# Kernel tuning notes

Measured on AMD Instinct MI355X. Metric: run time of the kernel, lower is better.

## Reference

```python
import jax, jax.numpy as jnp
import numpy as np


def setup_inputs() -> dict:
    key = jax.random.key(0)
    ks = jax.random.split(key, 6)
    B, V, T, Fin = 16, 12288, 4, 64
    Kv, Kt, Fout = 4, 4, 64
    NNZ = 9 * V  # ~8 neighbors + self loop per vertex (HEALPix)
    inputs = jax.random.normal(ks[0], (B, V, T, Fin), dtype=jnp.float32)
    std = np.sqrt(2.0 / (Fin * Kv * Kt))
    weight = jax.random.normal(ks[1], (Fin, Kv, Kt, Fout), dtype=jnp.float32) * std
    bias = jnp.zeros((Fout,), dtype=jnp.float32)
    lap_rows = jax.random.randint(ks[2], (NNZ,), 0, V, dtype=jnp.int32)
    lap_cols = jax.random.randint(ks[3], (NNZ,), 0, V, dtype=jnp.int32)
    # small values so the Chebyshev recurrence stays numerically tame
    lap_vals = jax.random.normal(ks[4], (NNZ,), dtype=jnp.float32) * 0.1
    return {"inputs": inputs, "weight": weight, "bias": bias,
            "lap_vals": lap_vals, "lap_rows": lap_rows, "lap_cols": lap_cols}


def _cheb_conv_temp(inputs, weight, lap_vals, lap_rows, lap_cols):
    B, V, T, Fin = inputs.shape
    Fin_w, Kv, Kt, Fout = weight.shape
    # x0: [V, T*Fin*B] matching torch permute(1,2,3,0).view
    x0 = jnp.transpose(inputs, (1, 2, 3, 0)).reshape(V, T * Fin * B)

    def spmm(x):  # sparse laplacian @ x via gather + segment_sum
        return jax.ops.segment_sum(lap_vals[:, None] * x[lap_cols], lap_rows,
                                   num_segments=V)

    xs = [x0]
    if Kv > 1:
        x1 = spmm(x0)
        xs.append(x1)
        for _ in range(2, Kv):
            x2 = 2.0 * spmm(x1) - x0
            xs.append(x2)
            x0, x1 = x1, x2
    x = jnp.stack(xs, axis=0).reshape(Kv, V, T, Fin, B)
    # contraction aligns flattened (Fin,Kv,T) of x with (Fin,Kv,Kt) of weight
    return jnp.einsum('kvtfb,fkto->bvo', x, weight)


def reference(inputs, weight, bias, lap_vals, lap_rows, lap_cols):
    out = _cheb_conv_temp(inputs, weight, lap_vals, lap_rows, lap_cols)
    return out + bias
```

## Files before the change

kernel.cpp:

```cpp
#include <hip/hip_runtime.h>

#define V_N 12288
#define B_N 16
#define TF_N 256
#define ROW2 1024
#define FOUT 64
#define TPB_TILES 4

typedef __attribute__((ext_vector_type(8))) short short8;
typedef __attribute__((ext_vector_type(4))) float f32x4;

__device__ __forceinline__ unsigned short f2bf(float x){
  unsigned u = __float_as_uint(x);
  return (unsigned short)((u + 0x7FFFu + ((u >> 16) & 1u)) >> 16);
}
__device__ __forceinline__ float bf2f(unsigned short h){
  return __uint_as_float(((unsigned)h) << 16);
}

__global__ void k_zero(int* __restrict__ p, int n){
  int i = blockIdx.x * 256 + threadIdx.x;
  if (i < n) p[i] = 0;
}

__global__ void k_hist(const int* __restrict__ rows, int* __restrict__ cnt, int nnz){
  int i = blockIdx.x * 256 + threadIdx.x;
  if (i < nnz) atomicAdd(&cnt[rows[i]], 1);
}

__global__ void k_scan(const int* __restrict__ cnt, int* __restrict__ rp){
  __shared__ int part[256];
  __shared__ int base[257];
  int t = threadIdx.x;
  const int per = V_N / 256;
  int4 c[12];
  #pragma unroll
  for (int i = 0; i < 12; ++i) c[i] = *(const int4*)(cnt + t * per + i * 4);
  int s = 0;
  #pragma unroll
  for (int i = 0; i < 12; ++i) s += c[i].x + c[i].y + c[i].z + c[i].w;
  part[t] = s;
  __syncthreads();
  if (t == 0){
    int run = 0;
    for (int i = 0; i < 256; ++i){ base[i] = run; run += part[i]; }
    base[256] = run;
  }
  __syncthreads();
  int run = base[t];
  #pragma unroll
  for (int i = 0; i < 12; ++i){
    int4 o;
    o.x = run; run += c[i].x;
    o.y = run; run += c[i].y;
    o.z = run; run += c[i].z;
    o.w = run; run += c[i].w;
    *(int4*)(rp + t * per + i * 4) = o;
  }
  if (t == 255) rp[V_N] = run;
}

__global__ void k_scatter(const int* __restrict__ rows, const int* __restrict__ cols,
                          const float* __restrict__ vals, const int* __restrict__ rp,
                          int* __restrict__ cur, int* __restrict__ cols_s,
                          float* __restrict__ vals_s, int nnz){
  int i = blockIdx.x * 256 + threadIdx.x;
  if (i < nnz){
    int r = rows[i];
    int pos = rp[r] + atomicAdd(&cur[r], 1);
    cols_s[pos] = cols[i];
    vals_s[pos] = vals[i];
  }
}

__global__ void k_convw(const float* __restrict__ w, unsigned short* __restrict__ wb){
  int i = blockIdx.x * 256 + threadIdx.x;
  int j = i & 7;
  int l = (i >> 3) & 63;
  int n = (i >> 9) & 3;
  int s = (i >> 11) & 7;
  int k = (i >> 14) & 3;
  int kk = s * 32 + ((l >> 4) << 3) + j;
  int t = kk >> 6, f = kk & 63;
  int o = (n << 4) + (l & 15);
  wb[i] = f2bf(w[((f * 4 + k) * 4 + t) * 64 + o]);
}

__global__ __launch_bounds__(256, 2) void k_proj(
                       const float* __restrict__ in, const unsigned short* __restrict__ wb,
                       unsigned short* __restrict__ y0, unsigned short* __restrict__ y1,
                       unsigned short* __restrict__ y2, unsigned short* __restrict__ y3){
  __shared__ unsigned short As[2][32 * 256];
  int t = threadIdx.x;
  int lane = t & 63;
  int k    = t >> 6;
  int colL = lane & 15, rg = lane >> 4;

  int tile0 = blockIdx.x * TPB_TILES;

  float4 r[8];
  {
    int vb = tile0 >> 4, b = tile0 & 15;
    const float* src = in + ((size_t)b * V_N + vb * 32) * TF_N;
    #pragma unroll
    for (int i = 0; i < 8; ++i) r[i] = *(const float4*)(src + i * 1024 + t * 4);
  }

  short8 W[8][4];
  {
    const unsigned short* wk = wb + k * 16384 + lane * 8;
    #pragma unroll
    for (int s = 0; s < 8; ++s)
      #pragma unroll
      for (int n = 0; n < 4; ++n)
        W[s][n] = *(const short8*)(wk + (((s * 4 + n)) << 9));
  }
  unsigned short* yk = (k == 0) ? y0 : (k == 1) ? y1 : (k == 2) ? y2 : y3;

  for (int ti = 0; ti < TPB_TILES; ++ti){
    int ft = tile0 + ti;
    char* lds = (char*)As[ti & 1];
    #pragma unroll
    for (int i = 0; i < 8; ++i){
      int flat = i * 1024 + t * 4;
      int row = flat >> 8;
      int c2  = (flat & 255) * 2;
      unsigned long long pk =  (unsigned long long)f2bf(r[i].x)
                            | ((unsigned long long)f2bf(r[i].y) << 16)
                            | ((unsigned long long)f2bf(r[i].z) << 32)
                            | ((unsigned long long)f2bf(r[i].w) << 48);
      *(unsigned long long*)(lds + ((row * 512 + c2) ^ ((row & 7) << 4))) = pk;
    }
    if (ti + 1 < TPB_TILES){
      int ft1 = ft + 1;
      int vb = ft1 >> 4, b = ft1 & 15;
      const float* src = in + ((size_t)b * V_N + vb * 32) * TF_N;
      #pragma unroll
      for (int i = 0; i < 8; ++i) r[i] = *(const float4*)(src + i * 1024 + t * 4);
    }
    __syncthreads();

    f32x4 acc[2][4];
    #pragma unroll
    for (int mt = 0; mt < 2; ++mt)
      #pragma unroll
      for (int n = 0; n < 4; ++n) acc[mt][n] = (f32x4){0.f, 0.f, 0.f, 0.f};

    #pragma unroll
    for (int s = 0; s < 8; ++s){
      int c2 = rg * 16 + s * 64;
      short8 a0 = *(const short8*)(lds + (( colL       * 512 + c2) ^ ((colL & 7) << 4)));
      short8 a1 = *(const short8*)(lds + (((16 + colL) * 512 + c2) ^ ((colL & 7) << 4)));
      #pragma unroll
      for (int n = 0; n < 4; ++n){
        acc[0][n] = __builtin_amdgcn_mfma_f32_16x16x32_bf16(a0, W[s][n], acc[0][n], 0, 0, 0);
        acc[1][n] = __builtin_amdgcn_mfma_f32_16x16x32_bf16(a1, W[s][n], acc[1][n], 0, 0, 0);
      }
    }
    {
      int vb = ft >> 4, b = ft & 15, v0 = vb * 32;
      #pragma unroll
      for (int mt = 0; mt < 2; ++mt)
        #pragma unroll
        for (int q = 0; q < 4; ++q){
          int v = v0 + mt * 16 + rg * 4 + q;
          unsigned lo = (unsigned)f2bf(acc[mt][0][q]) | ((unsigned)f2bf(acc[mt][1][q]) << 16);
          unsigned hi = (unsigned)f2bf(acc[mt][2][q]) | ((unsigned)f2bf(acc[mt][3][q]) << 16);
          uint2 pk = {lo, hi};
          *(uint2*)(yk + (size_t)v * ROW2 + b * 64 + colL * 4) = pk;
        }
    }
    __syncthreads();
  }
}

__global__ void k_spmm2(const unsigned short* __restrict__ src,
                        const unsigned short* __restrict__ addA,
                        const unsigned short* __restrict__ subB,
                        unsigned short* __restrict__ dst,
                        const int* __restrict__ rp, const int* __restrict__ cols,
                        const float* __restrict__ vals, float alpha){
  int lane = threadIdx.x & 63;
  int r = blockIdx.x * 4 + (threadIdx.x >> 6);
  int j0 = lane * 16;
  float acc[16];
  #pragma unroll
  for (int p = 0; p < 16; ++p) acc[p] = 0.f;
  int beg = rp[r], end = rp[r + 1];
  for (int i = beg; i < end; ++i){
    float val = vals[i];
    int c = cols[i];
    const unsigned short* srow = src + (size_t)c * ROW2 + j0;
    short8 a0 = *(const short8*)srow;
    short8 a1 = *(const short8*)(srow + 8);
    #pragma unroll
    for (int p = 0; p < 8; ++p) acc[p]     += val * bf2f((unsigned short)a0[p]);
    #pragma unroll
    for (int p = 0; p < 8; ++p) acc[p + 8] += val * bf2f((unsigned short)a1[p]);
  }
  const unsigned short* arow = addA + (size_t)r * ROW2 + j0;
  short8 q0 = *(const short8*)arow;
  short8 q1 = *(const short8*)(arow + 8);
  #pragma unroll
  for (int p = 0; p < 8; ++p) acc[p]     = alpha * acc[p]     + bf2f((unsigned short)q0[p]);
  #pragma unroll
  for (int p = 0; p < 8; ++p) acc[p + 8] = alpha * acc[p + 8] + bf2f((unsigned short)q1[p]);
  if (subB){
    const unsigned short* brow = subB + (size_t)r * ROW2 + j0;
    short8 s0 = *(const short8*)brow;
    short8 s1 = *(const short8*)(brow + 8);
    #pragma unroll
    for (int p = 0; p < 8; ++p) acc[p]     -= bf2f((unsigned short)s0[p]);
    #pragma unroll
    for (int p = 0; p < 8; ++p) acc[p + 8] -= bf2f((unsigned short)s1[p]);
  }
  unsigned short* drow = dst + (size_t)r * ROW2 + j0;
  short8 o0, o1;
  #pragma unroll
  for (int p = 0; p < 8; ++p) o0[p] = (short)f2bf(acc[p]);
  #pragma unroll
  for (int p = 0; p < 8; ++p) o1[p] = (short)f2bf(acc[p + 8]);
  *(short8*)drow = o0;
  *(short8*)(drow + 8) = o1;
}

__global__ void k_final(const unsigned short* __restrict__ src,
                        const unsigned short* __restrict__ y0,
                        const unsigned short* __restrict__ b2,
                        const float* __restrict__ bias,
                        float* __restrict__ out,
                        const int* __restrict__ rp, const int* __restrict__ cols,
                        const float* __restrict__ vals){
  int lane = threadIdx.x & 63;
  int v = blockIdx.x * 4 + (threadIdx.x >> 6);
  int j0 = lane * 16;
  float acc[16];
  #pragma unroll
  for (int p = 0; p < 16; ++p) acc[p] = 0.f;
  int beg = rp[v], end = rp[v + 1];
  for (int i = beg; i < end; ++i){
    float val = vals[i];
    int c = cols[i];
    const unsigned short* srow = src + (size_t)c * ROW2 + j0;
    short8 a0 = *(const short8*)srow;
    short8 a1 = *(const short8*)(srow + 8);
    #pragma unroll
    for (int p = 0; p < 8; ++p) acc[p]     += val * bf2f((unsigned short)a0[p]);
    #pragma unroll
    for (int p = 0; p < 8; ++p) acc[p + 8] += val * bf2f((unsigned short)a1[p]);
  }
  const unsigned short* yrow = y0 + (size_t)v * ROW2 + j0;
  const unsigned short* brow = b2 + (size_t)v * ROW2 + j0;
  short8 q0 = *(const short8*)yrow;
  short8 q1 = *(const short8*)(yrow + 8);
  short8 s0 = *(const short8*)brow;
  short8 s1 = *(const short8*)(brow + 8);
  #pragma unroll
  for (int p = 0; p < 8; ++p) acc[p]     += bf2f((unsigned short)q0[p]) - bf2f((unsigned short)s0[p]);
  #pragma unroll
  for (int p = 0; p < 8; ++p) acc[p + 8] += bf2f((unsigned short)q1[p]) - bf2f((unsigned short)s1[p]);
  int b = lane >> 2;
  int c0 = (lane & 3) * 4;
  float* obase = out + ((size_t)b * V_N + v) * FOUT;
  #pragma unroll
  for (int n = 0; n < 4; ++n){
    float4 bv = *(const float4*)(bias + n * 16 + c0);
    float4 w;
    w.x = acc[0 * 4 + n] + bv.x;
    w.y = acc[1 * 4 + n] + bv.y;
    w.z = acc[2 * 4 + n] + bv.z;
    w.w = acc[3 * 4 + n] + bv.w;
    *(float4*)(obase + n * 16 + c0) = w;
  }
}

extern "C" void kernel_launch(void* const* d_in, const int* in_sizes, int n_in,
                              void* d_out, int out_size, void* d_ws, size_t ws_size,
                              hipStream_t stream) {
  const float* inputs   = (const float*)d_in[0];
  const float* weight   = (const float*)d_in[1];
  const float* bias     = (const float*)d_in[2];
  const float* lap_vals = (const float*)d_in[3];
  const int*   lap_rows = (const int*)d_in[4];
  const int*   lap_cols = (const int*)d_in[5];
  float* out = (float*)d_out;
  int nnz = in_sizes[3];

  char* ws = (char*)d_ws;
  size_t off = 0;
  auto alloc = [&](size_t bytes) -> void* {
    void* p = ws + off;
    off += (bytes + 255) & ~(size_t)255;
    return p;
  };
  const size_t YB = (size_t)V_N * ROW2 * 2;
  unsigned short* y0 = (unsigned short*)alloc(YB);
  unsigned short* y1 = (unsigned short*)alloc(YB);
  unsigned short* y2 = (unsigned short*)alloc(YB);
  unsigned short* y3 = (unsigned short*)alloc(YB);
  unsigned short* c2 = (unsigned short*)alloc(YB);
  unsigned short* c1 = (unsigned short*)alloc(YB);
  unsigned short* wb = (unsigned short*)alloc(65536 * 2);
  int*   cnt   = (int*)alloc(V_N * 4);
  int*   cur   = (int*)alloc(V_N * 4);
  int*   rp    = (int*)alloc((V_N + 1) * 4);
  int*   colss = (int*)alloc((size_t)nnz * 4);
  float* valss = (float*)alloc((size_t)nnz * 4);

  k_zero<<<(2 * V_N + 255) / 256, 256, 0, stream>>>(cnt, 2 * V_N);
  k_hist<<<(nnz + 255) / 256, 256, 0, stream>>>(lap_rows, cnt, nnz);
  k_scan<<<1, 256, 0, stream>>>(cnt, rp);
  k_scatter<<<(nnz + 255) / 256, 256, 0, stream>>>(lap_rows, lap_cols, lap_vals, rp, cur,
                                                   colss, valss, nnz);
  k_convw<<<65536 / 256, 256, 0, stream>>>(weight, wb);
  k_proj<<<(V_N / 32) * B_N / TPB_TILES, 256, 0, stream>>>(inputs, wb, y0, y1, y2, y3);

  k_spmm2<<<V_N / 4, 256, 0, stream>>>(y3, y2, nullptr, c2, rp, colss, valss, 2.0f);
  k_spmm2<<<V_N / 4, 256, 0, stream>>>(c2, y1, y3, c1, rp, colss, valss, 2.0f);
  k_final<<<V_N / 4, 256, 0, stream>>>(c1, y0, c2, bias, out, rp, colss, valss);
}
```

Before: 215.2 us.

## Stream projection inputs directly into LDS and split SpMM rows across two waves

The projection kernel now copies fp32 input tiles from global memory straight into a double-buffered LDS array with the async global_load_lds builtin, using a pre-swizzled source address. The bf16 conversion moves to the LDS read side, which frees the staging registers and lets the next tile's load overlap the current MFMA work. The SpMM and final kernels give each row to two waves of 8 elements per lane instead of one wave of 16, doubling the grid to improve parallelism and latency hiding. The trade-offs are twice the LDS footprint (fp32 tiles), more conversion work per LDS read, and twice as many column and value index loads in the SpMM kernels.

```diff
diff --git a/kernel.cpp b/kernel.cpp
--- a/kernel.cpp
+++ b/kernel.cpp
@@ -90,7 +90,7 @@
                        const float* __restrict__ in, const unsigned short* __restrict__ wb,
                        unsigned short* __restrict__ y0, unsigned short* __restrict__ y1,
                        unsigned short* __restrict__ y2, unsigned short* __restrict__ y3){
-  __shared__ unsigned short As[2][32 * 256];
+  __shared__ float As[2][32 * 256];
   int t = threadIdx.x;
   int lane = t & 63;
   int k    = t >> 6;
@@ -98,12 +98,18 @@
 
   int tile0 = blockIdx.x * TPB_TILES;
 
-  float4 r[8];
   {
     int vb = tile0 >> 4, b = tile0 & 15;
-    const float* src = in + ((size_t)b * V_N + vb * 32) * TF_N;
-    #pragma unroll
-    for (int i = 0; i < 8; ++i) r[i] = *(const float4*)(src + i * 1024 + t * 4);
+    const char* gsrc = (const char*)(in + ((size_t)b * V_N + vb * 32) * TF_N);
+    char* lb = (char*)As[0];
+    #pragma unroll
+    for (int i = 0; i < 8; ++i){
+      int W = i * 4096 + t * 16;
+      int x = ((W >> 10) & 7) << 4;
+      __builtin_amdgcn_global_load_lds(
+          (const __attribute__((address_space(1))) unsigned int*)(gsrc + (W ^ x)),
+          (__attribute__((address_space(3))) unsigned int*)(lb + W), 16, 0, 0);
+    }
   }
 
   short8 W[8][4];
@@ -113,44 +119,53 @@
     for (int s = 0; s < 8; ++s)
       #pragma unroll
       for (int n = 0; n < 4; ++n)
-        W[s][n] = *(const short8*)(wk + (((s * 4 + n)) << 9));
+        W[s][n] = *(const short8*)(wk + ((s * 4 + n) << 9));
   }
   unsigned short* yk = (k == 0) ? y0 : (k == 1) ? y1 : (k == 2) ? y2 : y3;
 
   for (int ti = 0; ti < TPB_TILES; ++ti){
     int ft = tile0 + ti;
-    char* lds = (char*)As[ti & 1];
-    #pragma unroll
-    for (int i = 0; i < 8; ++i){
-      int flat = i * 1024 + t * 4;
-      int row = flat >> 8;
-      int c2  = (flat & 255) * 2;
-      unsigned long long pk =  (unsigned long long)f2bf(r[i].x)
-                            | ((unsigned long long)f2bf(r[i].y) << 16)
-                            | ((unsigned long long)f2bf(r[i].z) << 32)
-                            | ((unsigned long long)f2bf(r[i].w) << 48);
-      *(unsigned long long*)(lds + ((row * 512 + c2) ^ ((row & 7) << 4))) = pk;
-    }
+    __syncthreads();
     if (ti + 1 < TPB_TILES){
       int ft1 = ft + 1;
       int vb = ft1 >> 4, b = ft1 & 15;
-      const float* src = in + ((size_t)b * V_N + vb * 32) * TF_N;
-      #pragma unroll
-      for (int i = 0; i < 8; ++i) r[i] = *(const float4*)(src + i * 1024 + t * 4);
+      const char* gsrc = (const char*)(in + ((size_t)b * V_N + vb * 32) * TF_N);
+      char* lb = (char*)As[(ti + 1) & 1];
+      #pragma unroll
+      for (int i = 0; i < 8; ++i){
+        int W = i * 4096 + t * 16;
+        int x = ((W >> 10) & 7) << 4;
+        __builtin_amdgcn_global_load_lds(
+            (const __attribute__((address_space(1))) unsigned int*)(gsrc + (W ^ x)),
+            (__attribute__((address_space(3))) unsigned int*)(lb + W), 16, 0, 0);
+      }
     }
-    __syncthreads();
-
+
+    const char* lds = (const char*)As[ti & 1];
     f32x4 acc[2][4];
     #pragma unroll
     for (int mt = 0; mt < 2; ++mt)
       #pragma unroll
       for (int n = 0; n < 4; ++n) acc[mt][n] = (f32x4){0.f, 0.f, 0.f, 0.f};
 
+    int xr = (colL & 7) << 4;
     #pragma unroll
     for (int s = 0; s < 8; ++s){
-      int c2 = rg * 16 + s * 64;
-      short8 a0 = *(const short8*)(lds + (( colL       * 512 + c2) ^ ((colL & 7) << 4)));
-      short8 a1 = *(const short8*)(lds + (((16 + colL) * 512 + c2) ^ ((colL & 7) << 4)));
+      int B0 = colL * 1024 + rg * 32 + s * 128;
+      int B1 = (colL + 16) * 1024 + rg * 32 + s * 128;
+      float4 f00 = *(const float4*)(lds + ((B0) ^ xr));
+      float4 f01 = *(const float4*)(lds + ((B0 + 16) ^ xr));
+      float4 f10 = *(const float4*)(lds + ((B1) ^ xr));
+      float4 f11 = *(const float4*)(lds + ((B1 + 16) ^ xr));
+      short8 a0, a1;
+      a0[0] = (short)f2bf(f00.x); a0[1] = (short)f2bf(f00.y);
+      a0[2] = (short)f2bf(f00.z); a0[3] = (short)f2bf(f00.w);
+      a0[4] = (short)f2bf(f01.x); a0[5] = (short)f2bf(f01.y);
+      a0[6] = (short)f2bf(f01.z); a0[7] = (short)f2bf(f01.w);
+      a1[0] = (short)f2bf(f10.x); a1[1] = (short)f2bf(f10.y);
+      a1[2] = (short)f2bf(f10.z); a1[3] = (short)f2bf(f10.w);
+      a1[4] = (short)f2bf(f11.x); a1[5] = (short)f2bf(f11.y);
+      a1[6] = (short)f2bf(f11.z); a1[7] = (short)f2bf(f11.w);
       #pragma unroll
       for (int n = 0; n < 4; ++n){
         acc[0][n] = __builtin_amdgcn_mfma_f32_16x16x32_bf16(a0, W[s][n], acc[0][n], 0, 0, 0);
@@ -170,7 +185,6 @@
           *(uint2*)(yk + (size_t)v * ROW2 + b * 64 + colL * 4) = pk;
         }
     }
-    __syncthreads();
   }
 }
 
@@ -181,47 +195,32 @@
                         const int* __restrict__ rp, const int* __restrict__ cols,
                         const float* __restrict__ vals, float alpha){
   int lane = threadIdx.x & 63;
-  int r = blockIdx.x * 4 + (threadIdx.x >> 6);
-  int j0 = lane * 16;
-  float acc[16];
-  #pragma unroll
-  for (int p = 0; p < 16; ++p) acc[p] = 0.f;
+  int wave = threadIdx.x >> 6;
+  int r = blockIdx.x * 2 + (wave >> 1);
+  int j0 = (wave & 1) * 512 + lane * 8;
+  float acc[8];
+  #pragma unroll
+  for (int p = 0; p < 8; ++p) acc[p] = 0.f;
   int beg = rp[r], end = rp[r + 1];
   for (int i = beg; i < end; ++i){
     float val = vals[i];
     int c = cols[i];
-    const unsigned short* srow = src + (size_t)c * ROW2 + j0;
-    short8 a0 = *(const short8*)srow;
-    short8 a1 = *(const short8*)(srow + 8);
-    #pragma unroll
-    for (int p = 0; p < 8; ++p) acc[p]     += val * bf2f((unsigned short)a0[p]);
-    #pragma unroll
-    for (int p = 0; p < 8; ++p) acc[p + 8] += val * bf2f((unsigned short)a1[p]);
-  }
-  const unsigned short* arow = addA + (size_t)r * ROW2 + j0;
-  short8 q0 = *(const short8*)arow;
-  short8 q1 = *(const short8*)(arow + 8);
-  #pragma unroll
-  for (int p = 0; p < 8; ++p) acc[p]     = alpha * acc[p]     + bf2f((unsigned short)q0[p]);
-  #pragma unroll
-  for (int p = 0; p < 8; ++p) acc[p + 8] = alpha * acc[p + 8] + bf2f((unsigned short)q1[p]);
+    short8 a0 = *(const short8*)(src + (size_t)c * ROW2 + j0);
+    #pragma unroll
+    for (int p = 0; p < 8; ++p) acc[p] += val * bf2f((unsigned short)a0[p]);
+  }
+  short8 q0 = *(const short8*)(addA + (size_t)r * ROW2 + j0);
+  #pragma unroll
+  for (int p = 0; p < 8; ++p) acc[p] = alpha * acc[p] + bf2f((unsigned short)q0[p]);
   if (subB){
-    const unsigned short* brow = subB + (size_t)r * ROW2 + j0;
-    short8 s0 = *(const short8*)brow;
-    short8 s1 = *(const short8*)(brow + 8);
-    #pragma unroll
-    for (int p = 0; p < 8; ++p) acc[p]     -= bf2f((unsigned short)s0[p]);
-    #pragma unroll
-    for (int p = 0; p < 8; ++p) acc[p + 8] -= bf2f((unsigned short)s1[p]);
-  }
-  unsigned short* drow = dst + (size_t)r * ROW2 + j0;
-  short8 o0, o1;
+    short8 s0 = *(const short8*)(subB + (size_t)r * ROW2 + j0);
+    #pragma unroll
+    for (int p = 0; p < 8; ++p) acc[p] -= bf2f((unsigned short)s0[p]);
+  }
+  short8 o0;
   #pragma unroll
   for (int p = 0; p < 8; ++p) o0[p] = (short)f2bf(acc[p]);
-  #pragma unroll
-  for (int p = 0; p < 8; ++p) o1[p] = (short)f2bf(acc[p + 8]);
-  *(short8*)drow = o0;
-  *(short8*)(drow + 8) = o1;
+  *(short8*)(dst + (size_t)r * ROW2 + j0) = o0;
 }
 
 __global__ void k_final(const unsigned short* __restrict__ src,
@@ -232,45 +231,36 @@
                         const int* __restrict__ rp, const int* __restrict__ cols,
                         const float* __restrict__ vals){
   int lane = threadIdx.x & 63;
-  int v = blockIdx.x * 4 + (threadIdx.x >> 6);
-  int j0 = lane * 16;
-  float acc[16];
-  #pragma unroll
-  for (int p = 0; p < 16; ++p) acc[p] = 0.f;
+  int wave = threadIdx.x >> 6;
+  int v = blockIdx.x * 2 + (wave >> 1);
+  int jh = wave & 1;
+  int j0 = jh * 512 + lane * 8;
+  float acc[8];
+  #pragma unroll
+  for (int p = 0; p < 8; ++p) acc[p] = 0.f;
   int beg = rp[v], end = rp[v + 1];
   for (int i = beg; i < end; ++i){
     float val = vals[i];
     int c = cols[i];
-    const unsigned short* srow = src + (size_t)c * ROW2 + j0;
-    short8 a0 = *(const short8*)srow;
-    short8 a1 = *(const short8*)(srow + 8);
-    #pragma unroll
-    for (int p = 0; p < 8; ++p) acc[p]     += val * bf2f((unsigned short)a0[p]);
-    #pragma unroll
-    for (int p = 0; p < 8; ++p) acc[p + 8] += val * bf2f((unsigned short)a1[p]);
-  }
-  const unsigned short* yrow = y0 + (size_t)v * ROW2 + j0;
-  const unsigned short* brow = b2 + (size_t)v * ROW2 + j0;
-  short8 q0 = *(const short8*)yrow;
-  short8 q1 = *(const short8*)(yrow + 8);
-  short8 s0 = *(const short8*)brow;
-  short8 s1 = *(const short8*)(brow + 8);
-  #pragma unroll
-  for (int p = 0; p < 8; ++p) acc[p]     += bf2f((unsigned short)q0[p]) - bf2f((unsigned short)s0[p]);
-  #pragma unroll
-  for (int p = 0; p < 8; ++p) acc[p + 8] += bf2f((unsigned short)q1[p]) - bf2f((unsigned short)s1[p]);
-  int b = lane >> 2;
-  int c0 = (lane & 3) * 4;
-  float* obase = out + ((size_t)b * V_N + v) * FOUT;
+    short8 a0 = *(const short8*)(src + (size_t)c * ROW2 + j0);
+    #pragma unroll
+    for (int p = 0; p < 8; ++p) acc[p] += val * bf2f((unsigned short)a0[p]);
+  }
+  short8 q0 = *(const short8*)(y0 + (size_t)v * ROW2 + j0);
+  short8 s0 = *(const short8*)(b2 + (size_t)v * ROW2 + j0);
+  #pragma unroll
+  for (int p = 0; p < 8; ++p)
+    acc[p] += bf2f((unsigned short)q0[p]) - bf2f((unsigned short)s0[p]);
+  int bb = jh * 8 + (lane >> 3);
+  int cl2 = (lane & 7) * 2;
+  float* obase = out + ((size_t)bb * V_N + v) * FOUT;
   #pragma unroll
   for (int n = 0; n < 4; ++n){
-    float4 bv = *(const float4*)(bias + n * 16 + c0);
-    float4 w;
-    w.x = acc[0 * 4 + n] + bv.x;
-    w.y = acc[1 * 4 + n] + bv.y;
-    w.z = acc[2 * 4 + n] + bv.z;
-    w.w = acc[3 * 4 + n] + bv.w;
-    *(float4*)(obase + n * 16 + c0) = w;
+    int o = n * 16 + cl2;
+    float2 w;
+    w.x = acc[n]     + bias[o];
+    w.y = acc[4 + n] + bias[o + 1];
+    *(float2*)(obase + o) = w;
   }
 }
 
@@ -315,7 +305,7 @@
   k_convw<<<65536 / 256, 256, 0, stream>>>(weight, wb);
   k_proj<<<(V_N / 32) * B_N / TPB_TILES, 256, 0, stream>>>(inputs, wb, y0, y1, y2, y3);
 
-  k_spmm2<<<V_N / 4, 256, 0, stream>>>(y3, y2, nullptr, c2, rp, colss, valss, 2.0f);
-  k_spmm2<<<V_N / 4, 256, 0, stream>>>(c2, y1, y3, c1, rp, colss, valss, 2.0f);
-  k_final<<<V_N / 4, 256, 0, stream>>>(c1, y0, c2, bias, out, rp, colss, valss);
-}
+  k_spmm2<<<V_N / 2, 256, 0, stream>>>(y3, y2, nullptr, c2, rp, colss, valss, 2.0f);
+  k_spmm2<<<V_N / 2, 256, 0, stream>>>(c2, y1, y3, c1, rp, colss, valss, 2.0f);
+  k_final<<<V_N / 2, 256, 0, stream>>>(c1, y0, c2, bias, out, rp, colss, valss);
+}
```

Result: slower. 229.0 us (+6.4%).

## Split SpMM rows across 8 blocks with 2 bf16 elements per lane

Applied to the files above, without the earlier changes.

The SpMM and final kernels now split each 1024-wide bf16 row into 8 slices, so each wave handles 128 columns and each lane 2 elements. The grid grows 8x. This raises parallelism and cuts per-thread register use, hiding gather latency better. In exchange each lane does narrower 4-byte loads, the CSR indices and values are re-read 8 times, and the final output uses scalar scattered stores instead of float4.

```diff
diff --git a/kernel.cpp b/kernel.cpp
--- a/kernel.cpp
+++ b/kernel.cpp
@@ -113,7 +113,7 @@
     for (int s = 0; s < 8; ++s)
       #pragma unroll
       for (int n = 0; n < 4; ++n)
-        W[s][n] = *(const short8*)(wk + (((s * 4 + n)) << 9));
+        W[s][n] = *(const short8*)(wk + ((s * 4 + n) << 9));
   }
   unsigned short* yk = (k == 0) ? y0 : (k == 1) ? y1 : (k == 2) ? y2 : y3;
 
@@ -180,48 +180,30 @@
                         unsigned short* __restrict__ dst,
                         const int* __restrict__ rp, const int* __restrict__ cols,
                         const float* __restrict__ vals, float alpha){
+  int s = blockIdx.x & 7;
   int lane = threadIdx.x & 63;
-  int r = blockIdx.x * 4 + (threadIdx.x >> 6);
-  int j0 = lane * 16;
-  float acc[16];
-  #pragma unroll
-  for (int p = 0; p < 16; ++p) acc[p] = 0.f;
+  int wave = threadIdx.x >> 6;
+  int r = (blockIdx.x >> 3) * 4 + wave;
+  int j0 = s * 128 + lane * 2;
+  float a0 = 0.f, a1 = 0.f;
   int beg = rp[r], end = rp[r + 1];
   for (int i = beg; i < end; ++i){
     float val = vals[i];
     int c = cols[i];
-    const unsigned short* srow = src + (size_t)c * ROW2 + j0;
-    short8 a0 = *(const short8*)srow;
-    short8 a1 = *(const short8*)(srow + 8);
-    #pragma unroll
-    for (int p = 0; p < 8; ++p) acc[p]     += val * bf2f((unsigned short)a0[p]);
-    #pragma unroll
-    for (int p = 0; p < 8; ++p) acc[p + 8] += val * bf2f((unsigned short)a1[p]);
-  }
-  const unsigned short* arow = addA + (size_t)r * ROW2 + j0;
-  short8 q0 = *(const short8*)arow;
-  short8 q1 = *(const short8*)(arow + 8);
-  #pragma unroll
-  for (int p = 0; p < 8; ++p) acc[p]     = alpha * acc[p]     + bf2f((unsigned short)q0[p]);
-  #pragma unroll
-  for (int p = 0; p < 8; ++p) acc[p + 8] = alpha * acc[p + 8] + bf2f((unsigned short)q1[p]);
+    unsigned g = *(const unsigned*)(src + (size_t)c * ROW2 + j0);
+    a0 += val * bf2f((unsigned short)(g & 0xFFFF));
+    a1 += val * bf2f((unsigned short)(g >> 16));
+  }
+  unsigned q = *(const unsigned*)(addA + (size_t)r * ROW2 + j0);
+  a0 = alpha * a0 + bf2f((unsigned short)(q & 0xFFFF));
+  a1 = alpha * a1 + bf2f((unsigned short)(q >> 16));
   if (subB){
-    const unsigned short* brow = subB + (size_t)r * ROW2 + j0;
-    short8 s0 = *(const short8*)brow;
-    short8 s1 = *(const short8*)(brow + 8);
-    #pragma unroll
-    for (int p = 0; p < 8; ++p) acc[p]     -= bf2f((unsigned short)s0[p]);
-    #pragma unroll
-    for (int p = 0; p < 8; ++p) acc[p + 8] -= bf2f((unsigned short)s1[p]);
-  }
-  unsigned short* drow = dst + (size_t)r * ROW2 + j0;
-  short8 o0, o1;
-  #pragma unroll
-  for (int p = 0; p < 8; ++p) o0[p] = (short)f2bf(acc[p]);
-  #pragma unroll
-  for (int p = 0; p < 8; ++p) o1[p] = (short)f2bf(acc[p + 8]);
-  *(short8*)drow = o0;
-  *(short8*)(drow + 8) = o1;
+    unsigned sb = *(const unsigned*)(subB + (size_t)r * ROW2 + j0);
+    a0 -= bf2f((unsigned short)(sb & 0xFFFF));
+    a1 -= bf2f((unsigned short)(sb >> 16));
+  }
+  unsigned o = (unsigned)f2bf(a0) | ((unsigned)f2bf(a1) << 16);
+  *(unsigned*)(dst + (size_t)r * ROW2 + j0) = o;
 }
 
 __global__ void k_final(const unsigned short* __restrict__ src,
@@ -231,47 +213,33 @@
                         float* __restrict__ out,
                         const int* __restrict__ rp, const int* __restrict__ cols,
                         const float* __restrict__ vals){
+  int s = blockIdx.x & 7;
   int lane = threadIdx.x & 63;
-  int v = blockIdx.x * 4 + (threadIdx.x >> 6);
-  int j0 = lane * 16;
-  float acc[16];
-  #pragma unroll
-  for (int p = 0; p < 16; ++p) acc[p] = 0.f;
+  int wave = threadIdx.x >> 6;
+  int v = (blockIdx.x >> 3) * 4 + wave;
+  int j0 = s * 128 + lane * 2;
+  float a0 = 0.f, a1 = 0.f;
   int beg = rp[v], end = rp[v + 1];
   for (int i = beg; i < end; ++i){
     float val = vals[i];
     int c = cols[i];
-    const unsigned short* srow = src + (size_t)c * ROW2 + j0;
-    short8 a0 = *(const short8*)srow;
-    short8 a1 = *(const short8*)(srow + 8);
-    #pragma unroll
-    for (int p = 0; p < 8; ++p) acc[p]     += val * bf2f((unsigned short)a0[p]);
-    #pragma unroll
-    for (int p = 0; p < 8; ++p) acc[p + 8] += val * bf2f((unsigned short)a1[p]);
-  }
-  const unsigned short* yrow = y0 + (size_t)v * ROW2 + j0;
-  const unsigned short* brow = b2 + (size_t)v * ROW2 + j0;
-  short8 q0 = *(const short8*)yrow;
-  short8 q1 = *(const short8*)(yrow + 8);
-  short8 s0 = *(const short8*)brow;
-  short8 s1 = *(const short8*)(brow + 8);
-  #pragma unroll
-  for (int p = 0; p < 8; ++p) acc[p]     += bf2f((unsigned short)q0[p]) - bf2f((unsigned short)s0[p]);
-  #pragma unroll
-  for (int p = 0; p < 8; ++p) acc[p + 8] += bf2f((unsigned short)q1[p]) - bf2f((unsigned short)s1[p]);
-  int b = lane >> 2;
-  int c0 = (lane & 3) * 4;
+    unsigned g = *(const unsigned*)(src + (size_t)c * ROW2 + j0);
+    a0 += val * bf2f((unsigned short)(g & 0xFFFF));
+    a1 += val * bf2f((unsigned short)(g >> 16));
+  }
+  unsigned q = *(const unsigned*)(y0 + (size_t)v * ROW2 + j0);
+  unsigned sb = *(const unsigned*)(b2 + (size_t)v * ROW2 + j0);
+  a0 += bf2f((unsigned short)(q & 0xFFFF)) - bf2f((unsigned short)(sb & 0xFFFF));
+  a1 += bf2f((unsigned short)(q >> 16))    - bf2f((unsigned short)(sb >> 16));
+  int b   = 2 * s + (lane >> 5);
+  int jj  = (lane & 31) * 2;
+  int colL = jj >> 2;
+  int n0   = jj & 3;
+  int o0 = n0 * 16 + colL;
+  int o1 = (n0 + 1) * 16 + colL;
   float* obase = out + ((size_t)b * V_N + v) * FOUT;
-  #pragma unroll
-  for (int n = 0; n < 4; ++n){
-    float4 bv = *(const float4*)(bias + n * 16 + c0);
-    float4 w;
-    w.x = acc[0 * 4 + n] + bv.x;
-    w.y = acc[1 * 4 + n] + bv.y;
-    w.z = acc[2 * 4 + n] + bv.z;
-    w.w = acc[3 * 4 + n] + bv.w;
-    *(float4*)(obase + n * 16 + c0) = w;
-  }
+  obase[o0] = a0 + bias[o0];
+  obase[o1] = a1 + bias[o1];
 }
 
 extern "C" void kernel_launch(void* const* d_in, const int* in_sizes, int n_in,
@@ -315,7 +283,8 @@
   k_convw<<<65536 / 256, 256, 0, stream>>>(weight, wb);
   k_proj<<<(V_N / 32) * B_N / TPB_TILES, 256, 0, stream>>>(inputs, wb, y0, y1, y2, y3);
 
-  k_spmm2<<<V_N / 4, 256, 0, stream>>>(y3, y2, nullptr, c2, rp, colss, valss, 2.0f);
-  k_spmm2<<<V_N / 4, 256, 0, stream>>>(c2, y1, y3, c1, rp, colss, valss, 2.0f);
-  k_final<<<V_N / 4, 256, 0, stream>>>(c1, y0, c2, bias, out, rp, colss, valss);
-}
+  const int SG = (V_N / 4) * 8;
+  k_spmm2<<<SG, 256, 0, stream>>>(y3, y2, nullptr, c2, rp, colss, valss, 2.0f);
+  k_spmm2<<<SG, 256, 0, stream>>>(c2, y1, y3, c1, rp, colss, valss, 2.0f);
+  k_final<<<SG, 256, 0, stream>>>(c1, y0, c2, bias, out, rp, colss, valss);
+}
```

Result: slower. 352.0 us (+63.6%).
